# Performance work log

Measured on AMD Instinct MI355X. Metric: run time of the kernel, lower is better.

## Reference

```python
import jax, jax.numpy as jnp
import numpy as np

N, E, G, H, IN = 200000, 400000, 64, 128, 5
LN_EPS = 1e-5


def setup_inputs() -> dict:
    key = jax.random.key(0)
    ks = jax.random.split(key, 32)
    d = {}
    d["x"] = jax.random.normal(ks[0], (N, IN), jnp.float32)
    d["edge_index"] = jax.random.randint(ks[1], (2, E), 0, N, dtype=jnp.int32)
    d["edge_attr"] = jax.random.normal(ks[2], (E, 1), jnp.float32)
    d["batch"] = jnp.sort(jax.random.randint(ks[3], (N,), 0, G, dtype=jnp.int32))
    dims = [IN, H, H]
    i = 4
    names = [("ew", "eb", "w1_", "b1_", "w2_", "b2_", "g", "bt")]
    for l, din in enumerate(dims):
        d[f"ew{l}"] = jax.random.normal(ks[i], (1, din), jnp.float32); i += 1
        d[f"eb{l}"] = jnp.zeros((din,), jnp.float32)
        d[f"w1_{l}"] = jax.random.normal(ks[i], (din, H), jnp.float32) / np.sqrt(din); i += 1
        d[f"b1_{l}"] = jnp.zeros((H,), jnp.float32)
        d[f"w2_{l}"] = jax.random.normal(ks[i], (H, H), jnp.float32) / np.sqrt(H); i += 1
        d[f"b2_{l}"] = jnp.zeros((H,), jnp.float32)
        d[f"g{l}"] = jnp.ones((H,), jnp.float32)
        d[f"bt{l}"] = jnp.zeros((H,), jnp.float32)
    return d


def _gine_layer(x, src, dst, edge_attr, ew, eb, w1, b1, w2, b2, g, bt):
    # edge encoder: Linear(1, din)
    e = edge_attr @ ew + eb                       # [E, din]
    # GINEConv message: ReLU(x_j + e), aggregated (sum) at destination
    m = jax.nn.relu(x[src] + e)                   # [E, din]
    aggr = jax.ops.segment_sum(m, dst, num_segments=N)  # [N, din]
    h = x + aggr                                  # (1 + eps)*x with eps=0
    # GIN MLP: Linear -> ReLU -> Linear
    h = jax.nn.relu(h @ w1 + b1) @ w2 + b2        # [N, H]
    # LayerNorm
    mu = jnp.mean(h, axis=-1, keepdims=True)
    var = jnp.mean((h - mu) ** 2, axis=-1, keepdims=True)
    h = (h - mu) * jax.lax.rsqrt(var + LN_EPS) * g + bt
    return jax.nn.relu(h)


def reference(x, edge_index, edge_attr, batch,
              ew0, eb0, w1_0, b1_0, w2_0, b2_0, g0, bt0,
              ew1, eb1, w1_1, b1_1, w2_1, b2_1, g1, bt1,
              ew2, eb2, w1_2, b1_2, w2_2, b2_2, g2, bt2):
    src, dst = edge_index[0], edge_index[1]
    x = _gine_layer(x, src, dst, edge_attr, ew0, eb0, w1_0, b1_0, w2_0, b2_0, g0, bt0)
    x = _gine_layer(x, src, dst, edge_attr, ew1, eb1, w1_1, b1_1, w2_1, b2_1, g1, bt1)
    x = _gine_layer(x, src, dst, edge_attr, ew2, eb2, w1_2, b1_2, w2_2, b2_2, g2, bt2)
    # global pooling per graph
    add_pool = jax.ops.segment_sum(x, batch, num_segments=G)           # [G, H]
    counts = jax.ops.segment_sum(jnp.ones((N,), x.dtype), batch, num_segments=G)
    mean_pool = add_pool / jnp.maximum(counts, 1.0)[:, None]           # [G, H]
    return jnp.concatenate([mean_pool, add_pool], axis=1)              # [G, 2H]
```

## Files before the change

### kernel.cpp

```cpp
#include <hip/hip_runtime.h>

#define N_NODES 200000
#define N_EDGES 400000
#define N_GRAPHS 64
#define HDIM 128
#define INDIM 5
#define LN_EPS 1e-5f
#define LDA 140
#define NPBLK 64
#define BTH 512

typedef __attribute__((ext_vector_type(8))) short short8;
typedef __attribute__((ext_vector_type(4))) float f32x4;
typedef __attribute__((ext_vector_type(2))) float f32x2;

__device__ __forceinline__ unsigned short to_bf(float v) {
    unsigned u = __builtin_bit_cast(unsigned, v);
    return (unsigned short)((u + 0x7FFFu + ((u >> 16) & 1u)) >> 16);
}
__device__ __forceinline__ float bf_lo(unsigned w) { return __builtin_bit_cast(float, w << 16); }
__device__ __forceinline__ float bf_hi(unsigned w) { return __builtin_bit_cast(float, w & 0xFFFF0000u); }
__device__ __forceinline__ float bf2f(unsigned short h) { return __builtin_bit_cast(float, (unsigned)h << 16); }

__device__ __forceinline__ unsigned short cvt1_bf(float v) {
    unsigned r;
    asm("v_cvt_pk_bf16_f32 %0, %1, %1" : "=v"(r) : "v"(v));
    return (unsigned short)r;
}
__device__ __forceinline__ unsigned cvt2_bf(float lo, float hi) {
    unsigned r;
    asm("v_cvt_pk_bf16_f32 %0, %1, %2" : "=v"(r) : "v"(lo), "v"(hi));
    return r;
}
__device__ __forceinline__ f32x2 vmax0(f32x2 v) {
#if __has_builtin(__builtin_elementwise_max)
    return __builtin_elementwise_max(v, (f32x2)0.f);
#else
    v.x = fmaxf(v.x, 0.f);
    v.y = fmaxf(v.y, 0.f);
    return v;
#endif
}

#define GLOAD(p0, p1, srcrow)                                               \
    {                                                                       \
        const uint4* xs_ = (const uint4*)(xin + (size_t)(srcrow)*128 + c0); \
        p0 = xs_[0];                                                        \
        p1 = xs_[1];                                                        \
    }

#define GP2(wd, i0)                                \
    {                                              \
        float4 wb_ = ep[i0];                       \
        f32x2 xv_;                                 \
        xv_.x = bf_lo(wd);                         \
        xv_.y = bf_hi(wd);                         \
        f32x2 ew_, eb_;                            \
        ew_.x = wb_.x;                             \
        ew_.y = wb_.y;                             \
        eb_.x = wb_.z;                             \
        eb_.y = wb_.w;                             \
        f32x2 t_ = xv_ + eb_;                      \
        t_ = av2_ * ew_ + t_;                      \
        accv[i0] += vmax0(t_);                     \
    }

#define GPROC(p0, p1, a_)                                   \
    {                                                       \
        f32x2 av2_;                                         \
        av2_.x = (a_);                                      \
        av2_.y = (a_);                                      \
        GP2(p0.x, 0) GP2(p0.y, 1) GP2(p0.z, 2) GP2(p0.w, 3) \
        GP2(p1.x, 4) GP2(p1.y, 5) GP2(p1.z, 6) GP2(p1.w, 7) \
    }

#define GI2(wd, i0)                   \
    {                                 \
        accv[i0].x = bf_lo(wd);       \
        accv[i0].y = bf_hi(wd);       \
    }

#define GINIT(p0, p1)                                       \
    {                                                       \
        GI2(p0.x, 0) GI2(p0.y, 1) GI2(p0.z, 2) GI2(p0.w, 3) \
        GI2(p1.x, 4) GI2(p1.y, 5) GI2(p1.z, 6) GI2(p1.w, 7) \
    }


__global__ void hist_kernel(const int* __restrict__ ei, int* __restrict__ deg) {
    int e = blockIdx.x * blockDim.x + threadIdx.x;
    if (e < N_EDGES) atomicAdd(&deg[ei[N_EDGES + e]], 1);
}

#define SCAN_CHUNK 1024
#define SCAN_BLOCKS ((N_NODES + SCAN_CHUNK - 1) / SCAN_CHUNK)

__global__ __launch_bounds__(256) void scan_phaseA(const int* __restrict__ deg, int* __restrict__ bsums,
                                                   int* __restrict__ poolz) {
    if (blockIdx.x == 0) {
        for (int i = threadIdx.x; i < N_GRAPHS * HDIM + N_GRAPHS; i += 256) poolz[i] = 0;
    }
    __shared__ int red[256];
    int t = threadIdx.x;
    int base = blockIdx.x * SCAN_CHUNK + t * 4;
    int s = 0;
#pragma unroll
    for (int k = 0; k < 4; ++k) {
        int i = base + k;
        s += (i < N_NODES) ? deg[i] : 0;
    }
    red[t] = s;
    __syncthreads();
    for (int off = 128; off; off >>= 1) {
        if (t < off) red[t] += red[t + off];
        __syncthreads();
    }
    if (t == 0) bsums[blockIdx.x] = red[0];
}

__global__ __launch_bounds__(256) void scan_phaseB(int* __restrict__ bsums, int* __restrict__ row_ptr) {
    __shared__ int s[256];
    int t = threadIdx.x;
    int v = (t < SCAN_BLOCKS) ? bsums[t] : 0;
    s[t] = v;
    __syncthreads();
    for (int off = 1; off < 256; off <<= 1) {
        int add = (t >= off) ? s[t - off] : 0;
        __syncthreads();
        s[t] += add;
        __syncthreads();
    }
    if (t < SCAN_BLOCKS) bsums[t] = s[t] - v;
    if (t == SCAN_BLOCKS - 1) row_ptr[N_NODES] = s[t];
}

__global__ __launch_bounds__(256) void scan_phaseC(const int* __restrict__ deg,
                                                   const int* __restrict__ bsums,
                                                   int* __restrict__ row_ptr,
                                                   int* __restrict__ cursor) {
    __shared__ int ts[256];
    int t = threadIdx.x;
    int base = blockIdx.x * SCAN_CHUNK + t * 4;
    int v[4];
    int s = 0;
#pragma unroll
    for (int k = 0; k < 4; ++k) {
        int i = base + k;
        v[k] = (i < N_NODES) ? deg[i] : 0;
        s += v[k];
    }
    ts[t] = s;
    __syncthreads();
    for (int off = 1; off < 256; off <<= 1) {
        int add = (t >= off) ? ts[t - off] : 0;
        __syncthreads();
        ts[t] += add;
        __syncthreads();
    }
    int run = bsums[blockIdx.x] + ts[t] - s;
#pragma unroll
    for (int k = 0; k < 4; ++k) {
        int i = base + k;
        if (i < N_NODES) { row_ptr[i] = run; cursor[i] = 0; }
        run += v[k];
    }
}

#define SCATTER_BLOCKS ((N_EDGES + 255) / 256)

__global__ void scatter_pack(const int* __restrict__ ei, const float* __restrict__ ea,
                             const int* __restrict__ row_ptr, int* __restrict__ cursor,
                             int2* __restrict__ csr,
                             const float* __restrict__ s0, short* __restrict__ d0,
                             const float* __restrict__ s1, short* __restrict__ d1,
                             const float* __restrict__ s2, short* __restrict__ d2,
                             const float* __restrict__ s3, short* __restrict__ d3,
                             const float* __restrict__ s4, short* __restrict__ d4,
                             const float* __restrict__ s5, short* __restrict__ d5) {
    int b = blockIdx.x;
    if (b < SCATTER_BLOCKS) {
        int e = b * 256 + threadIdx.x;
        if (e >= N_EDGES) return;
        int d = ei[N_EDGES + e];
        int pos = atomicAdd(&cursor[d], 1);
        csr[row_ptr[d] + pos] = make_int2(ei[e], __float_as_int(ea[e]));
        return;
    }
    b -= SCATTER_BLOCKS;
    const float* W;
    short* D;
    int din, KP, b0;
    if (b < 16)       { W = s0; D = d0; din = 5;   KP = 32;  b0 = 0; }
    else if (b < 80)  { W = s1; D = d1; din = 128; KP = 128; b0 = 16; }
    else if (b < 144) { W = s2; D = d2; din = 128; KP = 128; b0 = 80; }
    else if (b < 208) { W = s3; D = d3; din = 128; KP = 128; b0 = 144; }
    else if (b < 272) { W = s4; D = d4; din = 128; KP = 128; b0 = 208; }
    else              { W = s5; D = d5; din = 128; KP = 128; b0 = 272; }
    int idx = (b - b0) * 256 + threadIdx.x;
    if (idx >= KP * 128) return;
    int j = idx & 7;
    int lane = (idx >> 3) & 63;
    int rest = idx >> 9;
    int KS = KP >> 5;
    int kstep = rest % KS;
    int tile = rest / KS;
    int k = kstep * 32 + ((lane >> 4) * 8) + j;
    int n = tile * 16 + (lane & 15);
    float v = (k < din) ? W[k * 128 + n] : 0.f;
    D[idx] = (short)to_bf(v);
}

template <int KP1, bool POOL>
__device__ __forceinline__ void mlp_tail8(
    unsigned short* A16, const int* bidx, float* sP, float* qP, int tid, int node0,
    const short* __restrict__ w1h, const float* __restrict__ b1,
    const short* __restrict__ w2h, const float* __restrict__ b2,
    const float* __restrict__ g, const float* __restrict__ bt,
    unsigned short* __restrict__ xout, float* __restrict__ pool, int* __restrict__ cnt) {
    int wv = tid >> 6, lane = tid & 63;
    int wg = wv & 3, half = wv >> 2;
    int mrow = lane & 15, q = lane >> 4;
    int arow = wg * 16 + mrow;

    const short8* w1p = (const short8*)w1h;
    const short8* w2p = (const short8*)w2h;

    f32x4 acc2[4];
#pragma unroll
    for (int t = 0; t < 4; ++t) acc2[t] = (f32x4){0.f, 0.f, 0.f, 0.f};
    constexpr int KS1 = KP1 / 32;
#pragma unroll
    for (int ks = 0; ks < KS1; ++ks) {
        short8 bh[4];
#pragma unroll
        for (int t = 0; t < 4; ++t) bh[t] = w1p[((size_t)(half * 4 + t) * KS1 + ks) * 64 + lane];
        short8 ah = *(const short8*)&A16[arow * LDA + ks * 32 + q * 8];
#pragma unroll
        for (int t = 0; t < 4; ++t)
            acc2[t] = __builtin_amdgcn_mfma_f32_16x16x32_bf16(ah, bh[t], acc2[t], 0, 0, 0);
    }
    __syncthreads();
    {
        float b1v[4];
#pragma unroll
        for (int t = 0; t < 4; ++t) b1v[t] = b1[(half * 4 + t) * 16 + mrow];
#pragma unroll
        for (int t = 0; t < 4; ++t)
#pragma unroll
            for (int r = 0; r < 4; ++r) {
                int rrow = wg * 16 + q * 4 + r;
                int col = (half * 4 + t) * 16 + mrow;
                A16[rrow * LDA + col] = cvt1_bf(fmaxf(acc2[t][r] + b1v[t], 0.f));
            }
    }
    __syncthreads();

#pragma unroll
    for (int t = 0; t < 4; ++t) acc2[t] = (f32x4){0.f, 0.f, 0.f, 0.f};
#pragma unroll
    for (int ks = 0; ks < 4; ++ks) {
        short8 bh[4];
#pragma unroll
        for (int t = 0; t < 4; ++t) bh[t] = w2p[((size_t)(half * 4 + t) * 4 + ks) * 64 + lane];
        short8 ah = *(const short8*)&A16[arow * LDA + ks * 32 + q * 8];
#pragma unroll
        for (int t = 0; t < 4; ++t)
            acc2[t] = __builtin_amdgcn_mfma_f32_16x16x32_bf16(ah, bh[t], acc2[t], 0, 0, 0);
    }

    float s4[4] = {0.f, 0.f, 0.f, 0.f}, q4[4] = {0.f, 0.f, 0.f, 0.f};
    {
        float b2v[4];
#pragma unroll
        for (int t = 0; t < 4; ++t) b2v[t] = b2[(half * 4 + t) * 16 + mrow];
#pragma unroll
        for (int t = 0; t < 4; ++t)
#pragma unroll
            for (int r = 0; r < 4; ++r) {
                float v = acc2[t][r] + b2v[t];
                acc2[t][r] = v;
                s4[r] += v;
                q4[r] += v * v;
            }
    }
#pragma unroll
    for (int m = 1; m <= 8; m <<= 1) {
#pragma unroll
        for (int r = 0; r < 4; ++r) {
            s4[r] += __shfl_xor(s4[r], m, 64);
            q4[r] += __shfl_xor(q4[r], m, 64);
        }
    }
    if (mrow == 0) {
#pragma unroll
        for (int r = 0; r < 4; ++r) {
            int rr = wg * 16 + q * 4 + r;
            sP[half * 64 + rr] = s4[r];
            qP[half * 64 + rr] = q4[r];
        }
    }
    __syncthreads();
    float mu[4], inv[4];
#pragma unroll
    for (int r = 0; r < 4; ++r) {
        int rr = wg * 16 + q * 4 + r;
        float s = sP[rr] + sP[64 + rr];
        float qq = qP[rr] + qP[64 + rr];
        mu[r] = s * (1.f / HDIM);
        float var = qq * (1.f / HDIM) - mu[r] * mu[r];
        inv[r] = rsqrtf(var + LN_EPS);
    }
    float gv[4], btv[4];
#pragma unroll
    for (int t = 0; t < 4; ++t) {
        gv[t] = g[(half * 4 + t) * 16 + mrow];
        btv[t] = bt[(half * 4 + t) * 16 + mrow];
    }

#pragma unroll
    for (int t = 0; t < 4; ++t)
#pragma unroll
        for (int r = 0; r < 4; ++r) {
            int rrow = wg * 16 + q * 4 + r;
            int col = (half * 4 + t) * 16 + mrow;
            float o = fmaxf((acc2[t][r] - mu[r]) * inv[r] * gv[t] + btv[t], 0.f);
            A16[rrow * LDA + col] = cvt1_bf(o);
        }
    __syncthreads();

    if (!POOL) {
        unsigned* xo = (unsigned*)xout;
#pragma unroll
        for (int i = 0; i < 8; ++i) {
            int idx = tid + BTH * i;
            int row = idx >> 6, w = idx & 63;
            xo[(size_t)(node0 + row) * 64 + w] = ((const unsigned*)&A16[row * LDA])[w];
        }
    } else {
        if (tid < 128) {
            int col = tid;
            float accp = 0.f;
            int cur = bidx[0];
            for (int r = 0; r < NPBLK; ++r) {
                int gi = bidx[r];
                if (gi != cur) {
                    unsafeAtomicAdd(&pool[cur * HDIM + col], accp);
                    accp = 0.f;
                    cur = gi;
                }
                accp += bf2f(A16[r * LDA + col]);
            }
            unsafeAtomicAdd(&pool[cur * HDIM + col], accp);
        } else if (tid == BTH - 1) {
            int cur = bidx[0], c = 0;
            for (int r = 0; r < NPBLK; ++r) {
                if (bidx[r] != cur) {
                    atomicAdd(&cnt[cur], c);
                    c = 0;
                    cur = bidx[r];
                }
                ++c;
            }
            atomicAdd(&cnt[cur], c);
        }
    }
}

template <bool POOL>
__global__ __launch_bounds__(BTH, 4) void layerH_fused(
    const unsigned short* __restrict__ xin, const int* __restrict__ row_ptr,
    const int2* __restrict__ csr,
    const float* __restrict__ ew, const float* __restrict__ eb,
    const short* __restrict__ w1h, const float* __restrict__ b1,
    const short* __restrict__ w2h, const float* __restrict__ b2,
    const float* __restrict__ g, const float* __restrict__ bt,
    unsigned short* __restrict__ xout,
    const int* __restrict__ batch, float* __restrict__ pool, int* __restrict__ cnt) {
    __shared__ __align__(16) unsigned short A16[NPBLK * LDA];
    __shared__ int bidx[NPBLK];
    __shared__ __align__(16) float4 eweb4[8 * 9];
    __shared__ float sP[128], qP[128];

    int tid = threadIdx.x;
    int node0 = blockIdx.x * NPBLK;

    if (tid < 64) {
        int qq = tid >> 3, ii = tid & 7, c = qq * 16 + ii * 2;
        eweb4[qq * 9 + ii] = make_float4(ew[c], ew[c + 1], eb[c], eb[c + 1]);
    }
    if (POOL && tid >= BTH - 64) bidx[tid - (BTH - 64)] = batch[node0 + tid - (BTH - 64)];

    int row = tid >> 3, qt = tid & 7, c0 = qt * 16;
    int node = node0 + row;

    const uint4* xn = (const uint4*)(xin + (size_t)node * 128 + c0);
    uint4 o0 = xn[0], o1 = xn[1];
    int beg = row_ptr[node], end = row_ptr[node + 1];

    uint4 va0, va1, vb0, vb1;
    float aA = 0.f, aB = 0.f;
    int2 rC = make_int2(0, 0), rD = rC, rE = rC, rF = rC;
    if (beg < end) {
        int2 r = csr[beg];
        aA = __int_as_float(r.y);
        GLOAD(va0, va1, r.x);
    }
    if (beg + 1 < end) {
        int2 r = csr[beg + 1];
        aB = __int_as_float(r.y);
        GLOAD(vb0, vb1, r.x);
    }
    if (beg + 2 < end) rC = csr[beg + 2];
    if (beg + 3 < end) rD = csr[beg + 3];
    if (beg + 4 < end) rE = csr[beg + 4];
    if (beg + 5 < end) rF = csr[beg + 5];
    __syncthreads();
    const float4* ep = (const float4*)eweb4 + qt * 9;

    f32x2 accv[8];
    GINIT(o0, o1);

    int e = beg;
    while (e + 3 < end) {
        GPROC(va0, va1, aA);
        GLOAD(va0, va1, rC.x);
        aA = __int_as_float(rC.y);
        GPROC(vb0, vb1, aB);
        GLOAD(vb0, vb1, rD.x);
        aB = __int_as_float(rD.y);
        rC = rE;
        rD = rF;
        int i6 = min(e + 6, end - 1);
        int i7 = min(e + 7, end - 1);
        rE = csr[i6];
        rF = csr[i7];
        e += 2;
    }
    if (e < end) GPROC(va0, va1, aA);
    if (e + 1 < end) GPROC(vb0, vb1, aB);
    if (e + 2 < end) {
        GLOAD(va0, va1, rC.x);
        GPROC(va0, va1, __int_as_float(rC.y));
    }

    uint2* Ar2 = (uint2*)&A16[row * LDA + c0];
#pragma unroll
    for (int k = 0; k < 4; ++k) {
        Ar2[k] = make_uint2(cvt2_bf(accv[2 * k].x, accv[2 * k].y),
                            cvt2_bf(accv[2 * k + 1].x, accv[2 * k + 1].y));
    }
    __syncthreads();

    mlp_tail8<128, POOL>(A16, bidx, sP, qP, tid, node0, w1h, b1, w2h, b2, g, bt, xout, pool, cnt);
}

__global__ __launch_bounds__(BTH, 4) void layer0_fused(
    const float* __restrict__ xinf, const int* __restrict__ row_ptr,
    const int2* __restrict__ csr,
    const float* __restrict__ ew, const float* __restrict__ eb,
    const short* __restrict__ w1h, const float* __restrict__ b1,
    const short* __restrict__ w2h, const float* __restrict__ b2,
    const float* __restrict__ g, const float* __restrict__ bt,
    unsigned short* __restrict__ xout) {
    __shared__ __align__(16) unsigned short A16[NPBLK * LDA];
    __shared__ float part[NPBLK][8][INDIM];
    __shared__ float sP[128], qP[128];

    int tid = threadIdx.x;
    int node0 = blockIdx.x * NPBLK;

    int row = tid >> 3, qt = tid & 7;
    int node = node0 + row;
    {
        float w[INDIM], b[INDIM], acc[INDIM];
#pragma unroll
        for (int j = 0; j < INDIM; ++j) {
            w[j] = ew[j];
            b[j] = eb[j];
            acc[j] = 0.f;
        }
        int beg = row_ptr[node], end = row_ptr[node + 1];
        int2 r;
        if (beg + qt < end) r = csr[beg + qt];
        for (int e = beg + qt; e < end; e += 8) {
            int2 rn = (e + 8 < end) ? csr[e + 8] : r;
            float a = __int_as_float(r.y);
#pragma unroll
            for (int j = 0; j < INDIM; ++j)
                acc[j] += fmaxf(fmaf(a, w[j], xinf[r.x * INDIM + j] + b[j]), 0.f);
            r = rn;
        }
#pragma unroll
        for (int j = 0; j < INDIM; ++j) part[row][qt][j] = acc[j];
    }
    __syncthreads();
    if (tid < NPBLK) {
#pragma unroll
        for (int j = 0; j < INDIM; ++j) {
            float v = xinf[(node0 + tid) * INDIM + j];
#pragma unroll
            for (int k = 0; k < 8; ++k) v += part[tid][k][j];
            A16[tid * LDA + j] = cvt1_bf(v);
        }
#pragma unroll
        for (int j = INDIM; j < 32; ++j) A16[tid * LDA + j] = 0;
    }
    __syncthreads();

    mlp_tail8<32, false>(A16, nullptr, sP, qP, tid, node0, w1h, b1, w2h, b2, g, bt, xout,
                         nullptr, nullptr);
}

__global__ void pool_final(const float* __restrict__ pool, const int* __restrict__ cnt,
                           float* __restrict__ out) {
    int g = blockIdx.x, j = threadIdx.x;
    float add = pool[g * HDIM + j];
    float c = (float)max(cnt[g], 1);
    out[g * (2 * HDIM) + j] = add / c;
    out[g * (2 * HDIM) + HDIM + j] = add;
}

extern "C" void kernel_launch(void* const* d_in, const int* in_sizes, int n_in,
                              void* d_out, int out_size, void* d_ws, size_t ws_size,
                              hipStream_t stream) {
    const float* x_in = (const float*)d_in[0];
    const int* ei = (const int*)d_in[1];
    const float* ea = (const float*)d_in[2];
    const int* batch = (const int*)d_in[3];
    const float* P[24];
    for (int i = 0; i < 24; ++i) P[i] = (const float*)d_in[4 + i];

    unsigned short* x_a = (unsigned short*)d_ws;
    unsigned short* x_b = x_a + (size_t)N_NODES * HDIM;
    float* pool = (float*)(x_b + (size_t)N_NODES * HDIM);
    int* cnt = (int*)(pool + N_GRAPHS * HDIM);
    int* deg = cnt + N_GRAPHS;
    int* cursor = deg + N_NODES;
    int* row_ptr = cursor + N_NODES;
    int* bsums = row_ptr + N_NODES + 1;
    int2* csr = (int2*)(bsums + 256);
    short* wp = (short*)(((uintptr_t)(csr + N_EDGES) + 15) & ~(uintptr_t)15);
    float* out = (float*)d_out;

    short *w1h[3], *w2h[3];
    for (int l = 0; l < 3; ++l) {
        w1h[l] = wp + (size_t)l * 32768;
        w2h[l] = w1h[l] + 16384;
    }

    hipMemsetAsync(deg, 0, N_NODES * sizeof(int), stream);

    hist_kernel<<<(N_EDGES + 255) / 256, 256, 0, stream>>>(ei, deg);
    scan_phaseA<<<SCAN_BLOCKS, 256, 0, stream>>>(deg, bsums, (int*)pool);
    scan_phaseB<<<1, 256, 0, stream>>>(bsums, row_ptr);
    scan_phaseC<<<SCAN_BLOCKS, 256, 0, stream>>>(deg, bsums, row_ptr, cursor);

    scatter_pack<<<SCATTER_BLOCKS + 336, 256, 0, stream>>>(
        ei, ea, row_ptr, cursor, csr,
        P[2], w1h[0], P[4], w2h[0],
        P[10], w1h[1], P[12], w2h[1],
        P[18], w1h[2], P[20], w2h[2]);

    layer0_fused<<<N_NODES / NPBLK, BTH, 0, stream>>>(
        x_in, row_ptr, csr, P[0], P[1],
        w1h[0], P[3], w2h[0], P[5], P[6], P[7], x_a);
    layerH_fused<false><<<N_NODES / NPBLK, BTH, 0, stream>>>(
        x_a, row_ptr, csr, P[8], P[9],
        w1h[1], P[11], w2h[1], P[13], P[14], P[15], x_b, nullptr, nullptr, nullptr);
    layerH_fused<true><<<N_NODES / NPBLK, BTH, 0, stream>>>(
        x_b, row_ptr, csr, P[16], P[17],
        w1h[2], P[19], w2h[2], P[21], P[22], P[23], nullptr, batch, pool, cnt);

    pool_final<<<N_GRAPHS, HDIM, 0, stream>>>(pool, cnt, out);
}
```

Baseline: 389.5 us.

## Split fused GINE layers into separate gather and MLP kernels

Each layer's fused gather+MLP kernel is split into a gather kernel that writes aggregated bf16 features to a workspace buffer and an MLP kernel that reads them back. The MLP kernel now uses 256 threads with each wave computing all 128 output columns, which removes the cross-wave LayerNorm reduction and several block barriers. Layer 0's gather is rewritten as one thread per node with software prefetching. The aim is to let the memory-bound gather and the MFMA-bound MLP each run at better occupancy, at the cost of an extra round trip of N×128 bf16 through global memory per layer.

```diff
diff --git a/kernel.cpp b/kernel.cpp
--- a/kernel.cpp
+++ b/kernel.cpp
@@ -8,7 +8,7 @@
 #define LN_EPS 1e-5f
 #define LDA 140
 #define NPBLK 64
-#define BTH 512
+#define GROWS 32
 
 typedef __attribute__((ext_vector_type(8))) short short8;
 typedef __attribute__((ext_vector_type(4))) float f32x4;
@@ -49,20 +49,20 @@
         p1 = xs_[1];                                                        \
     }
 
-#define GP2(wd, i0)                                \
-    {                                              \
-        float4 wb_ = ep[i0];                       \
-        f32x2 xv_;                                 \
-        xv_.x = bf_lo(wd);                         \
-        xv_.y = bf_hi(wd);                         \
-        f32x2 ew_, eb_;                            \
-        ew_.x = wb_.x;                             \
-        ew_.y = wb_.y;                             \
-        eb_.x = wb_.z;                             \
-        eb_.y = wb_.w;                             \
-        f32x2 t_ = xv_ + eb_;                      \
-        t_ = av2_ * ew_ + t_;                      \
-        accv[i0] += vmax0(t_);                     \
+#define GP2(wd, i0)                  \
+    {                                \
+        float4 wb_ = ep[i0];         \
+        f32x2 xv_;                   \
+        xv_.x = bf_lo(wd);           \
+        xv_.y = bf_hi(wd);           \
+        f32x2 ew_, eb_;              \
+        ew_.x = wb_.x;               \
+        ew_.y = wb_.y;               \
+        eb_.x = wb_.z;               \
+        eb_.y = wb_.w;               \
+        f32x2 t_ = xv_ + eb_;        \
+        t_ = av2_ * ew_ + t_;        \
+        accv[i0] += vmax0(t_);       \
     }
 
 #define GPROC(p0, p1, a_)                                   \
@@ -210,71 +210,239 @@
     D[idx] = (short)to_bf(v);
 }
 
+__global__ __launch_bounds__(256, 4) void gatherH(
+    const unsigned short* __restrict__ xin, const int* __restrict__ row_ptr,
+    const int2* __restrict__ csr,
+    const float* __restrict__ ew, const float* __restrict__ eb,
+    unsigned short* __restrict__ hout) {
+    __shared__ __align__(16) float4 eweb4[8 * 9];
+
+    int tid = threadIdx.x;
+    if (tid < 64) {
+        int qq = tid >> 3, ii = tid & 7, c = qq * 16 + ii * 2;
+        eweb4[qq * 9 + ii] = make_float4(ew[c], ew[c + 1], eb[c], eb[c + 1]);
+    }
+
+    int row = tid >> 3, qt = tid & 7, c0 = qt * 16;
+    int node = blockIdx.x * GROWS + row;
+
+    const uint4* xn = (const uint4*)(xin + (size_t)node * 128 + c0);
+    uint4 o0 = xn[0], o1 = xn[1];
+    int beg = row_ptr[node], end = row_ptr[node + 1];
+
+    uint4 va0, va1, vb0, vb1;
+    float aA = 0.f, aB = 0.f;
+    int2 rC = make_int2(0, 0), rD = rC, rE = rC, rF = rC;
+    if (beg < end) {
+        int2 r = csr[beg];
+        aA = __int_as_float(r.y);
+        GLOAD(va0, va1, r.x);
+    }
+    if (beg + 1 < end) {
+        int2 r = csr[beg + 1];
+        aB = __int_as_float(r.y);
+        GLOAD(vb0, vb1, r.x);
+    }
+    if (beg + 2 < end) rC = csr[beg + 2];
+    if (beg + 3 < end) rD = csr[beg + 3];
+    if (beg + 4 < end) rE = csr[beg + 4];
+    if (beg + 5 < end) rF = csr[beg + 5];
+    __syncthreads();
+    const float4* ep = (const float4*)eweb4 + qt * 9;
+
+    f32x2 accv[8];
+    GINIT(o0, o1);
+
+    int e = beg;
+    while (e + 3 < end) {
+        GPROC(va0, va1, aA);
+        GLOAD(va0, va1, rC.x);
+        aA = __int_as_float(rC.y);
+        GPROC(vb0, vb1, aB);
+        GLOAD(vb0, vb1, rD.x);
+        aB = __int_as_float(rD.y);
+        rC = rE;
+        rD = rF;
+        int i6 = min(e + 6, end - 1);
+        int i7 = min(e + 7, end - 1);
+        rE = csr[i6];
+        rF = csr[i7];
+        e += 2;
+    }
+    if (e < end) GPROC(va0, va1, aA);
+    if (e + 1 < end) GPROC(vb0, vb1, aB);
+    if (e + 2 < end) {
+        GLOAD(va0, va1, rC.x);
+        GPROC(va0, va1, __int_as_float(rC.y));
+    }
+
+    uint2* ho = (uint2*)(hout + (size_t)node * 128 + c0);
+#pragma unroll
+    for (int k = 0; k < 4; ++k) {
+        ho[k] = make_uint2(cvt2_bf(accv[2 * k].x, accv[2 * k].y),
+                           cvt2_bf(accv[2 * k + 1].x, accv[2 * k + 1].y));
+    }
+}
+
+__global__ __launch_bounds__(256, 4) void gather0(
+    const float* __restrict__ xinf, const int* __restrict__ row_ptr,
+    const int2* __restrict__ csr,
+    const float* __restrict__ ew, const float* __restrict__ eb,
+    unsigned short* __restrict__ h0) {
+    int node = blockIdx.x * 256 + threadIdx.x;
+    if (node >= N_NODES) return;
+
+    float w0 = ew[0], w1 = ew[1], w2 = ew[2], w3 = ew[3], w4 = ew[4];
+    float e0 = eb[0], e1 = eb[1], e2 = eb[2], e3 = eb[3], e4 = eb[4];
+    const float* xp = xinf + (size_t)node * INDIM;
+    float ac0 = xp[0], ac1 = xp[1], ac2 = xp[2], ac3 = xp[3], ac4 = xp[4];
+
+    int beg = row_ptr[node], end = row_ptr[node + 1];
+    float xa0, xa1, xa2, xa3, xa4, xb0, xb1, xb2, xb3, xb4;
+    float aA = 0.f, aB = 0.f;
+    int2 rC = make_int2(0, 0), rD = rC, rE = rC, rF = rC;
+#define L0X(a, b, c, d, f, src)                      \
+    {                                                \
+        const float* q_ = xinf + (size_t)(src)*INDIM; \
+        a = q_[0]; b = q_[1]; c = q_[2]; d = q_[3]; f = q_[4]; \
+    }
+#define P0X(a, b, c, d, f, av)                                   \
+    {                                                            \
+        ac0 += fmaxf(fmaf(av, w0, a + e0), 0.f);                 \
+        ac1 += fmaxf(fmaf(av, w1, b + e1), 0.f);                 \
+        ac2 += fmaxf(fmaf(av, w2, c + e2), 0.f);                 \
+        ac3 += fmaxf(fmaf(av, w3, d + e3), 0.f);                 \
+        ac4 += fmaxf(fmaf(av, w4, f + e4), 0.f);                 \
+    }
+    if (beg < end) {
+        int2 r = csr[beg];
+        aA = __int_as_float(r.y);
+        L0X(xa0, xa1, xa2, xa3, xa4, r.x);
+    }
+    if (beg + 1 < end) {
+        int2 r = csr[beg + 1];
+        aB = __int_as_float(r.y);
+        L0X(xb0, xb1, xb2, xb3, xb4, r.x);
+    }
+    if (beg + 2 < end) rC = csr[beg + 2];
+    if (beg + 3 < end) rD = csr[beg + 3];
+    if (beg + 4 < end) rE = csr[beg + 4];
+    if (beg + 5 < end) rF = csr[beg + 5];
+
+    int e = beg;
+    while (e + 3 < end) {
+        P0X(xa0, xa1, xa2, xa3, xa4, aA);
+        L0X(xa0, xa1, xa2, xa3, xa4, rC.x);
+        aA = __int_as_float(rC.y);
+        P0X(xb0, xb1, xb2, xb3, xb4, aB);
+        L0X(xb0, xb1, xb2, xb3, xb4, rD.x);
+        aB = __int_as_float(rD.y);
+        rC = rE;
+        rD = rF;
+        int i6 = min(e + 6, end - 1);
+        int i7 = min(e + 7, end - 1);
+        rE = csr[i6];
+        rF = csr[i7];
+        e += 2;
+    }
+    if (e < end) P0X(xa0, xa1, xa2, xa3, xa4, aA);
+    if (e + 1 < end) P0X(xb0, xb1, xb2, xb3, xb4, aB);
+    if (e + 2 < end) {
+        L0X(xa0, xa1, xa2, xa3, xa4, rC.x);
+        P0X(xa0, xa1, xa2, xa3, xa4, __int_as_float(rC.y));
+    }
+#undef L0X
+#undef P0X
+
+    unsigned* hp = (unsigned*)(h0 + (size_t)node * 32);
+    hp[0] = cvt2_bf(ac0, ac1);
+    hp[1] = cvt2_bf(ac2, ac3);
+    hp[2] = cvt2_bf(ac4, 0.f);
+#pragma unroll
+    for (int k = 3; k < 16; ++k) hp[k] = 0;
+}
+
 template <int KP1, bool POOL>
-__device__ __forceinline__ void mlp_tail8(
-    unsigned short* A16, const int* bidx, float* sP, float* qP, int tid, int node0,
+__global__ __launch_bounds__(256, 4) void mlpH(
+    const unsigned short* __restrict__ hin,
     const short* __restrict__ w1h, const float* __restrict__ b1,
     const short* __restrict__ w2h, const float* __restrict__ b2,
     const float* __restrict__ g, const float* __restrict__ bt,
-    unsigned short* __restrict__ xout, float* __restrict__ pool, int* __restrict__ cnt) {
+    unsigned short* __restrict__ xout,
+    const int* __restrict__ batch, float* __restrict__ pool, int* __restrict__ cnt) {
+    __shared__ __align__(16) unsigned short A16[NPBLK * LDA];
+    __shared__ int bidx[NPBLK];
+
+    int tid = threadIdx.x;
+    int node0 = blockIdx.x * NPBLK;
+
+    constexpr int DW2 = KP1 / 4;
+    constexpr int ITER = NPBLK * DW2 / 256;
+#pragma unroll
+    for (int i = 0; i < ITER; ++i) {
+        int idx = tid + 256 * i;
+        int row = idx / DW2, w2 = idx % DW2;
+        ((uint2*)&A16[row * LDA])[w2] =
+            ((const uint2*)(hin + (size_t)(node0 + row) * KP1))[w2];
+    }
+    if (POOL && tid >= 64 && tid < 128) bidx[tid - 64] = batch[node0 + tid - 64];
+    __syncthreads();
+
     int wv = tid >> 6, lane = tid & 63;
-    int wg = wv & 3, half = wv >> 2;
     int mrow = lane & 15, q = lane >> 4;
-    int arow = wg * 16 + mrow;
+    int arow = wv * 16 + mrow;
 
     const short8* w1p = (const short8*)w1h;
     const short8* w2p = (const short8*)w2h;
 
-    f32x4 acc2[4];
-#pragma unroll
-    for (int t = 0; t < 4; ++t) acc2[t] = (f32x4){0.f, 0.f, 0.f, 0.f};
+    f32x4 acc2[8];
+#pragma unroll
+    for (int t = 0; t < 8; ++t) acc2[t] = (f32x4){0.f, 0.f, 0.f, 0.f};
     constexpr int KS1 = KP1 / 32;
 #pragma unroll
     for (int ks = 0; ks < KS1; ++ks) {
-        short8 bh[4];
-#pragma unroll
-        for (int t = 0; t < 4; ++t) bh[t] = w1p[((size_t)(half * 4 + t) * KS1 + ks) * 64 + lane];
+        short8 bh[8];
+#pragma unroll
+        for (int t = 0; t < 8; ++t) bh[t] = w1p[((size_t)t * KS1 + ks) * 64 + lane];
         short8 ah = *(const short8*)&A16[arow * LDA + ks * 32 + q * 8];
 #pragma unroll
-        for (int t = 0; t < 4; ++t)
+        for (int t = 0; t < 8; ++t)
             acc2[t] = __builtin_amdgcn_mfma_f32_16x16x32_bf16(ah, bh[t], acc2[t], 0, 0, 0);
     }
-    __syncthreads();
     {
-        float b1v[4];
-#pragma unroll
-        for (int t = 0; t < 4; ++t) b1v[t] = b1[(half * 4 + t) * 16 + mrow];
-#pragma unroll
-        for (int t = 0; t < 4; ++t)
+        float b1v[8];
+#pragma unroll
+        for (int t = 0; t < 8; ++t) b1v[t] = b1[t * 16 + mrow];
+#pragma unroll
+        for (int t = 0; t < 8; ++t)
 #pragma unroll
             for (int r = 0; r < 4; ++r) {
-                int rrow = wg * 16 + q * 4 + r;
-                int col = (half * 4 + t) * 16 + mrow;
+                int rrow = wv * 16 + q * 4 + r;
+                int col = t * 16 + mrow;
                 A16[rrow * LDA + col] = cvt1_bf(fmaxf(acc2[t][r] + b1v[t], 0.f));
             }
     }
-    __syncthreads();
-
-#pragma unroll
-    for (int t = 0; t < 4; ++t) acc2[t] = (f32x4){0.f, 0.f, 0.f, 0.f};
+
+#pragma unroll
+    for (int t = 0; t < 8; ++t) acc2[t] = (f32x4){0.f, 0.f, 0.f, 0.f};
 #pragma unroll
     for (int ks = 0; ks < 4; ++ks) {
-        short8 bh[4];
-#pragma unroll
-        for (int t = 0; t < 4; ++t) bh[t] = w2p[((size_t)(half * 4 + t) * 4 + ks) * 64 + lane];
+        short8 bh[8];
+#pragma unroll
+        for (int t = 0; t < 8; ++t) bh[t] = w2p[((size_t)t * 4 + ks) * 64 + lane];
         short8 ah = *(const short8*)&A16[arow * LDA + ks * 32 + q * 8];
 #pragma unroll
-        for (int t = 0; t < 4; ++t)
+        for (int t = 0; t < 8; ++t)
             acc2[t] = __builtin_amdgcn_mfma_f32_16x16x32_bf16(ah, bh[t], acc2[t], 0, 0, 0);
     }
 
     float s4[4] = {0.f, 0.f, 0.f, 0.f}, q4[4] = {0.f, 0.f, 0.f, 0.f};
     {
-        float b2v[4];
-#pragma unroll
-        for (int t = 0; t < 4; ++t) b2v[t] = b2[(half * 4 + t) * 16 + mrow];
-#pragma unroll
-        for (int t = 0; t < 4; ++t)
+        float b2v[8];
+#pragma unroll
+        for (int t = 0; t < 8; ++t) b2v[t] = b2[t * 16 + mrow];
+#pragma unroll
+        for (int t = 0; t < 8; ++t)
 #pragma unroll
             for (int r = 0; r < 4; ++r) {
                 float v = acc2[t][r] + b2v[t];
@@ -291,38 +459,26 @@
             q4[r] += __shfl_xor(q4[r], m, 64);
         }
     }
-    if (mrow == 0) {
+    float mu[4], inv[4];
+#pragma unroll
+    for (int r = 0; r < 4; ++r) {
+        mu[r] = s4[r] * (1.f / HDIM);
+        float var = q4[r] * (1.f / HDIM) - mu[r] * mu[r];
+        inv[r] = rsqrtf(var + LN_EPS);
+    }
+    float gv[8], btv[8];
+#pragma unroll
+    for (int t = 0; t < 8; ++t) {
+        gv[t] = g[t * 16 + mrow];
+        btv[t] = bt[t * 16 + mrow];
+    }
+
+#pragma unroll
+    for (int t = 0; t < 8; ++t)
 #pragma unroll
         for (int r = 0; r < 4; ++r) {
-            int rr = wg * 16 + q * 4 + r;
-            sP[half * 64 + rr] = s4[r];
-            qP[half * 64 + rr] = q4[r];
-        }
-    }
-    __syncthreads();
-    float mu[4], inv[4];
-#pragma unroll
-    for (int r = 0; r < 4; ++r) {
-        int rr = wg * 16 + q * 4 + r;
-        float s = sP[rr] + sP[64 + rr];
-        float qq = qP[rr] + qP[64 + rr];
-        mu[r] = s * (1.f / HDIM);
-        float var = qq * (1.f / HDIM) - mu[r] * mu[r];
-        inv[r] = rsqrtf(var + LN_EPS);
-    }
-    float gv[4], btv[4];
-#pragma unroll
-    for (int t = 0; t < 4; ++t) {
-        gv[t] = g[(half * 4 + t) * 16 + mrow];
-        btv[t] = bt[(half * 4 + t) * 16 + mrow];
-    }
-
-#pragma unroll
-    for (int t = 0; t < 4; ++t)
-#pragma unroll
-        for (int r = 0; r < 4; ++r) {
-            int rrow = wg * 16 + q * 4 + r;
-            int col = (half * 4 + t) * 16 + mrow;
+            int rrow = wv * 16 + q * 4 + r;
+            int col = t * 16 + mrow;
             float o = fmaxf((acc2[t][r] - mu[r]) * inv[r] * gv[t] + btv[t], 0.f);
             A16[rrow * LDA + col] = cvt1_bf(o);
         }
@@ -331,8 +487,8 @@
     if (!POOL) {
         unsigned* xo = (unsigned*)xout;
 #pragma unroll
-        for (int i = 0; i < 8; ++i) {
-            int idx = tid + BTH * i;
+        for (int i = 0; i < 16; ++i) {
+            int idx = tid + 256 * i;
             int row = idx >> 6, w = idx & 63;
             xo[(size_t)(node0 + row) * 64 + w] = ((const unsigned*)&A16[row * LDA])[w];
         }
@@ -351,7 +507,7 @@
                 accp += bf2f(A16[r * LDA + col]);
             }
             unsafeAtomicAdd(&pool[cur * HDIM + col], accp);
-        } else if (tid == BTH - 1) {
+        } else if (tid == 255) {
             int cur = bidx[0], c = 0;
             for (int r = 0; r < NPBLK; ++r) {
                 if (bidx[r] != cur) {
@@ -366,151 +522,6 @@
     }
 }
 
-template <bool POOL>
-__global__ __launch_bounds__(BTH, 4) void layerH_fused(
-    const unsigned short* __restrict__ xin, const int* __restrict__ row_ptr,
-    const int2* __restrict__ csr,
-    const float* __restrict__ ew, const float* __restrict__ eb,
-    const short* __restrict__ w1h, const float* __restrict__ b1,
-    const short* __restrict__ w2h, const float* __restrict__ b2,
-    const float* __restrict__ g, const float* __restrict__ bt,
-    unsigned short* __restrict__ xout,
-    const int* __restrict__ batch, float* __restrict__ pool, int* __restrict__ cnt) {
-    __shared__ __align__(16) unsigned short A16[NPBLK * LDA];
-    __shared__ int bidx[NPBLK];
-    __shared__ __align__(16) float4 eweb4[8 * 9];
-    __shared__ float sP[128], qP[128];
-
-    int tid = threadIdx.x;
-    int node0 = blockIdx.x * NPBLK;
-
-    if (tid < 64) {
-        int qq = tid >> 3, ii = tid & 7, c = qq * 16 + ii * 2;
-        eweb4[qq * 9 + ii] = make_float4(ew[c], ew[c + 1], eb[c], eb[c + 1]);
-    }
-    if (POOL && tid >= BTH - 64) bidx[tid - (BTH - 64)] = batch[node0 + tid - (BTH - 64)];
-
-    int row = tid >> 3, qt = tid & 7, c0 = qt * 16;
-    int node = node0 + row;
-
-    const uint4* xn = (const uint4*)(xin + (size_t)node * 128 + c0);
-    uint4 o0 = xn[0], o1 = xn[1];
-    int beg = row_ptr[node], end = row_ptr[node + 1];
-
-    uint4 va0, va1, vb0, vb1;
-    float aA = 0.f, aB = 0.f;
-    int2 rC = make_int2(0, 0), rD = rC, rE = rC, rF = rC;
-    if (beg < end) {
-        int2 r = csr[beg];
-        aA = __int_as_float(r.y);
-        GLOAD(va0, va1, r.x);
-    }
-    if (beg + 1 < end) {
-        int2 r = csr[beg + 1];
-        aB = __int_as_float(r.y);
-        GLOAD(vb0, vb1, r.x);
-    }
-    if (beg + 2 < end) rC = csr[beg + 2];
-    if (beg + 3 < end) rD = csr[beg + 3];
-    if (beg + 4 < end) rE = csr[beg + 4];
-    if (beg + 5 < end) rF = csr[beg + 5];
-    __syncthreads();
-    const float4* ep = (const float4*)eweb4 + qt * 9;
-
-    f32x2 accv[8];
-    GINIT(o0, o1);
-
-    int e = beg;
-    while (e + 3 < end) {
-        GPROC(va0, va1, aA);
-        GLOAD(va0, va1, rC.x);
-        aA = __int_as_float(rC.y);
-        GPROC(vb0, vb1, aB);
-        GLOAD(vb0, vb1, rD.x);
-        aB = __int_as_float(rD.y);
-        rC = rE;
-        rD = rF;
-        int i6 = min(e + 6, end - 1);
-        int i7 = min(e + 7, end - 1);
-        rE = csr[i6];
-        rF = csr[i7];
-        e += 2;
-    }
-    if (e < end) GPROC(va0, va1, aA);
-    if (e + 1 < end) GPROC(vb0, vb1, aB);
-    if (e + 2 < end) {
-        GLOAD(va0, va1, rC.x);
-        GPROC(va0, va1, __int_as_float(rC.y));
-    }
-
-    uint2* Ar2 = (uint2*)&A16[row * LDA + c0];
-#pragma unroll
-    for (int k = 0; k < 4; ++k) {
-        Ar2[k] = make_uint2(cvt2_bf(accv[2 * k].x, accv[2 * k].y),
-                            cvt2_bf(accv[2 * k + 1].x, accv[2 * k + 1].y));
-    }
-    __syncthreads();
-
-    mlp_tail8<128, POOL>(A16, bidx, sP, qP, tid, node0, w1h, b1, w2h, b2, g, bt, xout, pool, cnt);
-}
-
-__global__ __launch_bounds__(BTH, 4) void layer0_fused(
-    const float* __restrict__ xinf, const int* __restrict__ row_ptr,
-    const int2* __restrict__ csr,
-    const float* __restrict__ ew, const float* __restrict__ eb,
-    const short* __restrict__ w1h, const float* __restrict__ b1,
-    const short* __restrict__ w2h, const float* __restrict__ b2,
-    const float* __restrict__ g, const float* __restrict__ bt,
-    unsigned short* __restrict__ xout) {
-    __shared__ __align__(16) unsigned short A16[NPBLK * LDA];
-    __shared__ float part[NPBLK][8][INDIM];
-    __shared__ float sP[128], qP[128];
-
-    int tid = threadIdx.x;
-    int node0 = blockIdx.x * NPBLK;
-
-    int row = tid >> 3, qt = tid & 7;
-    int node = node0 + row;
-    {
-        float w[INDIM], b[INDIM], acc[INDIM];
-#pragma unroll
-        for (int j = 0; j < INDIM; ++j) {
-            w[j] = ew[j];
-            b[j] = eb[j];
-            acc[j] = 0.f;
-        }
-        int beg = row_ptr[node], end = row_ptr[node + 1];
-        int2 r;
-        if (beg + qt < end) r = csr[beg + qt];
-        for (int e = beg + qt; e < end; e += 8) {
-            int2 rn = (e + 8 < end) ? csr[e + 8] : r;
-            float a = __int_as_float(r.y);
-#pragma unroll
-            for (int j = 0; j < INDIM; ++j)
-                acc[j] += fmaxf(fmaf(a, w[j], xinf[r.x * INDIM + j] + b[j]), 0.f);
-            r = rn;
-        }
-#pragma unroll
-        for (int j = 0; j < INDIM; ++j) part[row][qt][j] = acc[j];
-    }
-    __syncthreads();
-    if (tid < NPBLK) {
-#pragma unroll
-        for (int j = 0; j < INDIM; ++j) {
-            float v = xinf[(node0 + tid) * INDIM + j];
-#pragma unroll
-            for (int k = 0; k < 8; ++k) v += part[tid][k][j];
-            A16[tid * LDA + j] = cvt1_bf(v);
-        }
-#pragma unroll
-        for (int j = INDIM; j < 32; ++j) A16[tid * LDA + j] = 0;
-    }
-    __syncthreads();
-
-    mlp_tail8<32, false>(A16, nullptr, sP, qP, tid, node0, w1h, b1, w2h, b2, g, bt, xout,
-                         nullptr, nullptr);
-}
-
 __global__ void pool_final(const float* __restrict__ pool, const int* __restrict__ cnt,
                            float* __restrict__ out) {
     int g = blockIdx.x, j = threadIdx.x;
@@ -532,7 +543,9 @@
 
     unsigned short* x_a = (unsigned short*)d_ws;
     unsigned short* x_b = x_a + (size_t)N_NODES * HDIM;
-    float* pool = (float*)(x_b + (size_t)N_NODES * HDIM);
+    unsigned short* hbuf = x_b + (size_t)N_NODES * HDIM;
+    unsigned short* h0 = hbuf;
+    float* pool = (float*)(hbuf + (size_t)N_NODES * HDIM);
     int* cnt = (int*)(pool + N_GRAPHS * HDIM);
     int* deg = cnt + N_GRAPHS;
     int* cursor = deg + N_NODES;
@@ -561,15 +574,17 @@
         P[10], w1h[1], P[12], w2h[1],
         P[18], w1h[2], P[20], w2h[2]);
 
-    layer0_fused<<<N_NODES / NPBLK, BTH, 0, stream>>>(
-        x_in, row_ptr, csr, P[0], P[1],
-        w1h[0], P[3], w2h[0], P[5], P[6], P[7], x_a);
-    layerH_fused<false><<<N_NODES / NPBLK, BTH, 0, stream>>>(
-        x_a, row_ptr, csr, P[8], P[9],
-        w1h[1], P[11], w2h[1], P[13], P[14], P[15], x_b, nullptr, nullptr, nullptr);
-    layerH_fused<true><<<N_NODES / NPBLK, BTH, 0, stream>>>(
-        x_b, row_ptr, csr, P[16], P[17],
-        w1h[2], P[19], w2h[2], P[21], P[22], P[23], nullptr, batch, pool, cnt);
+    gather0<<<(N_NODES + 255) / 256, 256, 0, stream>>>(x_in, row_ptr, csr, P[0], P[1], h0);
+    mlpH<32, false><<<N_NODES / NPBLK, 256, 0, stream>>>(
+        h0, w1h[0], P[3], w2h[0], P[5], P[6], P[7], x_a, nullptr, nullptr, nullptr);
+
+    gatherH<<<N_NODES / GROWS, 256, 0, stream>>>(x_a, row_ptr, csr, P[8], P[9], hbuf);
+    mlpH<128, false><<<N_NODES / NPBLK, 256, 0, stream>>>(
+        hbuf, w1h[1], P[11], w2h[1], P[13], P[14], P[15], x_b, nullptr, nullptr, nullptr);
+
+    gatherH<<<N_NODES / GROWS, 256, 0, stream>>>(x_b, row_ptr, csr, P[16], P[17], hbuf);
+    mlpH<128, true><<<N_NODES / NPBLK, 256, 0, stream>>>(
+        hbuf, w1h[2], P[19], w2h[2], P[21], P[22], P[23], nullptr, batch, pool, cnt);
 
     pool_final<<<N_GRAPHS, HDIM, 0, stream>>>(pool, cnt, out);
 }
```

Result: faster. 381.8 us (-2.0%).
